# Optimization experiments

Measured on AMD Instinct MI355X. Metric: run time of the kernel, lower is better.

## Reference

```python
import jax, jax.numpy as jnp
import numpy as np
import math

L, E, H, T, B, V = 6, 768, 12, 1024, 4, 256
HS = E // H


def _ln(x, w, b, eps=1e-5):
    mu = jnp.mean(x, axis=-1, keepdims=True)
    var = jnp.mean((x - mu) ** 2, axis=-1, keepdims=True)
    return (x - mu) * jax.lax.rsqrt(var + eps) * w + b


def setup_inputs() -> dict:
    key = jax.random.key(0)
    ks = jax.random.split(key, 12)
    std = 0.02
    inp = {
        "idx": jax.random.randint(ks[0], (B, T), 0, V, dtype=jnp.int64),
        "tok_emb": jax.random.normal(ks[1], (V, E), jnp.float32) * std,
        "pos_emb": jnp.zeros((1, T, E), jnp.float32),
        "ln1_w": jnp.ones((L, E), jnp.float32),
        "ln1_b": jnp.zeros((L, E), jnp.float32),
        "Wq": jax.random.normal(ks[2], (L, E, E), jnp.float32) * std,
        "bq": jnp.zeros((L, E), jnp.float32),
        "Wk": jax.random.normal(ks[3], (L, E, E), jnp.float32) * std,
        "bk": jnp.zeros((L, E), jnp.float32),
        "Wv": jax.random.normal(ks[4], (L, E, E), jnp.float32) * std,
        "bv": jnp.zeros((L, E), jnp.float32),
        "Wp": jax.random.normal(ks[5], (L, E, E), jnp.float32) * std,
        "bp": jnp.zeros((L, E), jnp.float32),
        "ln2_w": jnp.ones((L, E), jnp.float32),
        "ln2_b": jnp.zeros((L, E), jnp.float32),
        "W1": jax.random.normal(ks[6], (L, E, 4 * E), jnp.float32) * std,
        "b1": jnp.zeros((L, 4 * E), jnp.float32),
        "W2": jax.random.normal(ks[7], (L, 4 * E, E), jnp.float32) * std,
        "b2": jnp.zeros((L, E), jnp.float32),
        "lnf_w": jnp.ones((E,), jnp.float32),
        "lnf_b": jnp.zeros((E,), jnp.float32),
        "lm_head": jax.random.normal(ks[8], (E, V), jnp.float32) * std,
    }
    return inp


def reference(idx, tok_emb, pos_emb, ln1_w, ln1_b, Wq, bq, Wk, bk, Wv, bv, Wp, bp,
              ln2_w, ln2_b, W1, b1, W2, b2, lnf_w, lnf_b, lm_head):
    Bc, Tc = idx.shape
    causal = jnp.tril(jnp.ones((Tc, Tc), bool))  # [T,T]
    scale = 1.0 / math.sqrt(HS)
    x = tok_emb[idx] + pos_emb[:, :Tc, :]  # [B,T,E]
    for l in range(L):
        h = _ln(x, ln1_w[l], ln1_b[l])
        q = (h @ Wq[l] + bq[l]).reshape(Bc, Tc, H, HS).transpose(0, 2, 1, 3)
        k = (h @ Wk[l] + bk[l]).reshape(Bc, Tc, H, HS).transpose(0, 2, 1, 3)
        v = (h @ Wv[l] + bv[l]).reshape(Bc, Tc, H, HS).transpose(0, 2, 1, 3)
        att = jnp.einsum('bhtd,bhsd->bhts', q, k) * scale  # [B,H,T,T]
        att = jnp.where(causal, att, -jnp.inf)
        att = jax.nn.softmax(att, axis=-1)
        y = jnp.einsum('bhts,bhsd->bhtd', att, v)
        y = y.transpose(0, 2, 1, 3).reshape(Bc, Tc, E)
        x = x + (y @ Wp[l] + bp[l])
        h2 = _ln(x, ln2_w[l], ln2_b[l])
        m = jax.nn.gelu(h2 @ W1[l] + b1[l], approximate=False)
        x = x + (m @ W2[l] + b2[l])
    x = _ln(x, lnf_w, lnf_b)
    logits = x @ lm_head  # [B,T,V]
    return logits
```

## Files before the change

kernel.cpp:

```cpp
#include <hip/hip_runtime.h>

#define L_ 6
#define E_ 768
#define H_ 12
#define T_ 1024
#define B_ 4
#define V_ 256
#define M_ (B_*T_)
#define E4_ (4*E_)
#define QKVN (3*E_)
#define NZ_ 4

typedef __bf16 bf16;
typedef __bf16 bf16x8 __attribute__((ext_vector_type(8)));
typedef __bf16 bf16x4 __attribute__((ext_vector_type(4)));
typedef float f32x4 __attribute__((ext_vector_type(4)));

#define GF_GELU     1
#define GF_BIAS_EXT 16
#define GF_PART     32

__device__ __forceinline__ float ldf(const void* p, size_t i, int f32m) {
    return f32m ? ((const float*)p)[i] : (float)((const bf16*)p)[i];
}

__device__ __forceinline__ void async_cp16(const void* g, void* l) {
    __builtin_amdgcn_global_load_lds(
        (__attribute__((address_space(1))) void*)g,
        (__attribute__((address_space(3))) void*)l, 16, 0, 0);
}

__device__ __forceinline__ float exp2_hw(float x) {
    float r; asm("v_exp_f32 %0, %1" : "=v"(r) : "v"(x)); return r;
}

__global__ __launch_bounds__(256) void k_probe(const void* __restrict__ tok,
    const void* __restrict__ idxp, int* __restrict__ dm)
{
    __shared__ int sc1, sc2;
    if (threadIdx.x == 0) { sc1 = 0; sc2 = 0; }
    __syncthreads();
    const bf16* tb = (const bf16*)tok;
    int c1 = 0;
    for (int i = threadIdx.x; i < 4096; i += 256) {
        float v = (float)tb[2 * i];
        if (!(fabsf(v) < 100.f)) c1++;
    }
    const int* ip = (const int*)idxp;
    int c2 = 0;
    for (int i = threadIdx.x; i < 1024; i += 256)
        if (ip[2 * i + 1] != 0) c2++;
    atomicAdd(&sc1, c1);
    atomicAdd(&sc2, c2);
    __syncthreads();
    if (threadIdx.x == 0) { dm[0] = (sc1 > 400) ? 1 : 0; dm[1] = (sc2 < 100) ? 1 : 0; }
}

__global__ __launch_bounds__(256) void k_embed(const void* __restrict__ idxp,
    const void* __restrict__ tok, const void* __restrict__ pos,
    float* __restrict__ x, const int* __restrict__ dm)
{
    int f32m = dm[0], i64m = dm[1];
    int bt = blockIdx.x;
    int t  = bt & (T_ - 1);
    int id = i64m ? ((const int*)idxp)[2 * bt] : ((const int*)idxp)[bt];
    float* xo = x + (size_t)bt * E_;
    for (int e = threadIdx.x; e < E_; e += 256)
        xo[e] = ldf(tok, (size_t)id * E_ + e, f32m) + ldf(pos, (size_t)t * E_ + e, f32m);
}

__global__ __launch_bounds__(256) void k_ln(const float* __restrict__ x,
    const void* __restrict__ w, const void* __restrict__ b, size_t wboff,
    bf16* __restrict__ out, const int* __restrict__ dm)
{
    int f32m = dm[0];
    int row = blockIdx.x;
    int tid = threadIdx.x;
    const float* xr = x + (size_t)row * E_;
    float v0 = xr[tid], v1 = xr[tid + 256], v2 = xr[tid + 512];
    float s  = v0 + v1 + v2;
    float s2 = v0*v0 + v1*v1 + v2*v2;
    for (int off = 32; off; off >>= 1) {
        s  += __shfl_xor(s,  off);
        s2 += __shfl_xor(s2, off);
    }
    __shared__ float ls[4], ls2[4];
    int wave = tid >> 6;
    if ((tid & 63) == 0) { ls[wave] = s; ls2[wave] = s2; }
    __syncthreads();
    s  = ls[0] + ls[1] + ls[2] + ls[3];
    s2 = ls2[0] + ls2[1] + ls2[2] + ls2[3];
    float mu  = s * (1.0f / E_);
    float var = s2 * (1.0f / E_) - mu * mu;
    float rs  = rsqrtf(var + 1e-5f);
    bf16* o = out + (size_t)row * E_;
    o[tid]       = (bf16)(((v0 - mu) * rs) * ldf(w, wboff + tid,       f32m) + ldf(b, wboff + tid,       f32m));
    o[tid + 256] = (bf16)(((v1 - mu) * rs) * ldf(w, wboff + tid + 256, f32m) + ldf(b, wboff + tid + 256, f32m));
    o[tid + 512] = (bf16)(((v2 - mu) * rs) * ldf(w, wboff + tid + 512, f32m) + ldf(b, wboff + tid + 512, f32m));
}

__global__ __launch_bounds__(256) void k_red_ln(float* __restrict__ x,
    const float* __restrict__ part,
    const void* __restrict__ gb, size_t gboff,
    const void* __restrict__ w, const void* __restrict__ b, size_t wboff,
    bf16* __restrict__ out, const int* __restrict__ dm)
{
    const size_t PSTR = (size_t)M_ * E_;
    int f32m = dm[0];
    int row = blockIdx.x;
    int tid = threadIdx.x;
    float* xr = x + (size_t)row * E_;
    const float* pr = part + (size_t)row * E_;
    float v[3];
    #pragma unroll
    for (int j = 0; j < 3; j++) {
        int c = tid + j * 256;
        float acc = xr[c];
        #pragma unroll
        for (int z = 0; z < NZ_; z++) acc += pr[(size_t)z * PSTR + c];
        acc += ldf(gb, gboff + c, f32m);
        v[j] = acc;
        xr[c] = acc;
    }
    float s  = v[0] + v[1] + v[2];
    float s2 = v[0]*v[0] + v[1]*v[1] + v[2]*v[2];
    for (int off = 32; off; off >>= 1) {
        s  += __shfl_xor(s,  off);
        s2 += __shfl_xor(s2, off);
    }
    __shared__ float ls[4], ls2[4];
    int wave = tid >> 6;
    if ((tid & 63) == 0) { ls[wave] = s; ls2[wave] = s2; }
    __syncthreads();
    s  = ls[0] + ls[1] + ls[2] + ls[3];
    s2 = ls2[0] + ls2[1] + ls2[2] + ls2[3];
    float mu  = s * (1.0f / E_);
    float var = s2 * (1.0f / E_) - mu * mu;
    float rs  = rsqrtf(var + 1e-5f);
    bf16* o = out + (size_t)row * E_;
    #pragma unroll
    for (int j = 0; j < 3; j++) {
        int c = tid + j * 256;
        o[c] = (bf16)(((v[j] - mu) * rs) * ldf(w, wboff + c, f32m) + ldf(b, wboff + c, f32m));
    }
}

__global__ __launch_bounds__(256) void k_transpose(const void* __restrict__ in, size_t inoff,
    bf16* __restrict__ out, int R, int C, const int* __restrict__ dm)
{
    int f32m = dm[0];
    __shared__ bf16 tile[32][33];
    int r0 = blockIdx.x * 32, c0 = blockIdx.y * 32;
    int tx = threadIdx.x & 31, ty = threadIdx.x >> 5;
    #pragma unroll
    for (int i = 0; i < 4; i++)
        tile[ty + 8*i][tx] = (bf16)ldf(in, inoff + (size_t)(r0 + ty + 8*i) * C + (c0 + tx), f32m);
    __syncthreads();
    #pragma unroll
    for (int i = 0; i < 4; i++)
        out[(size_t)(c0 + ty + 8*i) * R + (r0 + tx)] = tile[tx][ty + 8*i];
}

__global__ __launch_bounds__(256) void k_transpose3(const void* __restrict__ a,
    const void* __restrict__ b, const void* __restrict__ c, size_t inoff,
    bf16* __restrict__ out, int R, int C, const int* __restrict__ dm)
{
    int f32m = dm[0];
    const void* in = (blockIdx.z == 0) ? a : ((blockIdx.z == 1) ? b : c);
    bf16* o = out + (size_t)blockIdx.z * R * C;
    __shared__ bf16 tile[32][33];
    int r0 = blockIdx.x * 32, c0 = blockIdx.y * 32;
    int tx = threadIdx.x & 31, ty = threadIdx.x >> 5;
    #pragma unroll
    for (int i = 0; i < 4; i++)
        tile[ty + 8*i][tx] = (bf16)ldf(in, inoff + (size_t)(r0 + ty + 8*i) * C + (c0 + tx), f32m);
    __syncthreads();
    #pragma unroll
    for (int i = 0; i < 4; i++)
        o[(size_t)(c0 + ty + 8*i) * R + (r0 + tx)] = tile[tx][ty + 8*i];
}

__global__ __launch_bounds__(256) void k_cat3(const void* __restrict__ a,
    const void* __restrict__ b, const void* __restrict__ c, size_t voff,
    bf16* __restrict__ o, const int* __restrict__ dm)
{
    int f32m = dm[0];
    int i = blockIdx.x * 256 + threadIdx.x;
    float v = (i < E_) ? ldf(a, voff + i, f32m)
            : ((i < 2*E_) ? ldf(b, voff + i - E_, f32m) : ldf(c, voff + i - 2*E_, f32m));
    o[i] = (bf16)v;
}

__global__ __launch_bounds__(256) void k_cast_red(const float* __restrict__ in,
    void* __restrict__ out, const int* __restrict__ dm)
{
    const size_t S = (size_t)M_ * V_ / 4;
    size_t i = (size_t)blockIdx.x * 256 + threadIdx.x;
    const f32x4* p = (const f32x4*)in;
    f32x4 v = p[i];
    v += p[S + i];
    v += p[2*S + i];
    v += p[3*S + i];
    if (dm[0]) {
        ((f32x4*)out)[i] = v;
    } else {
        bf16x4 o;
        #pragma unroll
        for (int j = 0; j < 4; j++) o[j] = (bf16)v[j];
        ((bf16x4*)out)[i] = o;
    }
}

__global__ __launch_bounds__(256) void k_gemm(const bf16* __restrict__ A,
    const bf16* __restrict__ BT, const void* __restrict__ bias, size_t boff,
    void* __restrict__ outp, int M, int N, int K, int flags, const int* __restrict__ dm)
{
    int f32m = dm[0];
    __shared__ __attribute__((aligned(16))) bf16 As[128 * 64];
    __shared__ __attribute__((aligned(16))) bf16 Bs[128 * 64];
    int tid = threadIdx.x;
    int bn0 = blockIdx.x * 128, bm0 = blockIdx.y * 128;
    int kz = blockIdx.z;
    int Ks = K / gridDim.z;
    int kbeg = kz * Ks, kend = kbeg + Ks;
    int wave = tid >> 6, lane = tid & 63, quad = lane >> 4, l16 = lane & 15;
    int wr = wave >> 1, wc = wave & 1;

    int st_col = 8 * ((lane & 7) ^ (lane >> 3));
    int st_row_base = wave * 32 + (lane >> 3);

    f32x4 acc[4][4];
    #pragma unroll
    for (int i = 0; i < 4; i++)
        #pragma unroll
        for (int j = 0; j < 4; j++)
            acc[i][j] = (f32x4){0.f, 0.f, 0.f, 0.f};

    int sw = l16 & 7;
    for (int k0 = kbeg; k0 < kend; k0 += 64) {
        #pragma unroll
        for (int i = 0; i < 4; i++) {
            int row = st_row_base + i * 8;
            const bf16* ga = A  + (size_t)(bm0 + row) * K + k0 + st_col;
            const bf16* gb = BT + (size_t)(bn0 + row) * K + k0 + st_col;
            bf16* la = As + (size_t)(wave * 256 + i * 64) * 8;
            bf16* lb = Bs + (size_t)(wave * 256 + i * 64) * 8;
            async_cp16(ga, la);
            async_cp16(gb, lb);
        }
        __syncthreads();
        #pragma unroll
        for (int ks = 0; ks < 2; ks++) {
            bf16x8 af[4], bfr[4];
            #pragma unroll
            for (int mi = 0; mi < 4; mi++) {
                int row = wr*64 + mi*16 + l16;
                int kgs = (4*ks + quad) ^ sw;
                af[mi] = *(const bf16x8*)&As[row*64 + kgs*8];
            }
            #pragma unroll
            for (int ni = 0; ni < 4; ni++) {
                int row = wc*64 + ni*16 + l16;
                int kgs = (4*ks + quad) ^ sw;
                bfr[ni] = *(const bf16x8*)&Bs[row*64 + kgs*8];
            }
            #pragma unroll
            for (int mi = 0; mi < 4; mi++)
                #pragma unroll
                for (int ni = 0; ni < 4; ni++)
                    acc[mi][ni] = __builtin_amdgcn_mfma_f32_16x16x32_bf16(af[mi], bfr[ni], acc[mi][ni], 0, 0, 0);
        }
        __syncthreads();
    }

    float* pout = (float*)outp + (size_t)kz * M * N;
    #pragma unroll
    for (int mi = 0; mi < 4; mi++) {
        #pragma unroll
        for (int ni = 0; ni < 4; ni++) {
            int col = bn0 + wc*64 + ni*16 + l16;
            float bv = 0.f;
            if (bias)
                bv = (flags & GF_BIAS_EXT) ? ldf(bias, boff + col, f32m)
                                           : (float)((const bf16*)bias)[col];
            #pragma unroll
            for (int r = 0; r < 4; r++) {
                int row = bm0 + wr*64 + mi*16 + quad*4 + r;
                float val = acc[mi][ni][r] + bv;
                if (flags & GF_GELU) val = 0.5f * val * (1.f + erff(val * 0.70710678118f));
                size_t oidx = (size_t)row * N + col;
                if (flags & GF_PART) pout[oidx] = val;
                else                 ((bf16*)outp)[oidx] = (bf16)val;
            }
        }
    }
}

__device__ __forceinline__ void attn_qk_softmax2(
    const bf16x8 qf[2], f32x4 OT[4], float& m_ln, float& l_ln,
    const bf16* __restrict__ Kbuf, bf16 (*Ps)[72],
    int wave, int quad, int l16, int s0, int qt0, bool diag)
{
    f32x4 S[4];
    #pragma unroll
    for (int i = 0; i < 4; i++) S[i] = (f32x4){0.f, 0.f, 0.f, 0.f};
    #pragma unroll
    for (int ks = 0; ks < 2; ks++)
        #pragma unroll
        for (int ni = 0; ni < 4; ni++) {
            int kg = (ks*4 + quad) ^ (l16 & 7);
            bf16x8 kf = *(const bf16x8*)&Kbuf[(ni*16 + l16)*64 + kg*8];
            S[ni] = __builtin_amdgcn_mfma_f32_16x16x32_bf16(kf, qf[ks], S[ni], 0, 0, 0);
        }
    const float SC = 0.18033688011112042f;
    if (diag) {
        int qr = qt0 + wave*16 + l16;
        #pragma unroll
        for (int ni = 0; ni < 4; ni++)
            #pragma unroll
            for (int r = 0; r < 4; r++) {
                int scol = s0 + ni*16 + quad*4 + r;
                S[ni][r] = (scol > qr) ? -1e30f : S[ni][r] * SC;
            }
    } else {
        #pragma unroll
        for (int ni = 0; ni < 4; ni++)
            #pragma unroll
            for (int r = 0; r < 4; r++) S[ni][r] *= SC;
    }
    float tn[4];
    #pragma unroll
    for (int ni = 0; ni < 4; ni++)
        tn[ni] = fmaxf(fmaxf(S[ni][0], S[ni][1]), fmaxf(S[ni][2], S[ni][3]));
    float tm = fmaxf(fmaxf(tn[0], tn[1]), fmaxf(tn[2], tn[3]));
    tm = fmaxf(tm, __shfl_xor(tm, 16));
    tm = fmaxf(tm, __shfl_xor(tm, 32));
    float mnew = fmaxf(m_ln, tm);
    float alpha = exp2_hw(m_ln - mnew);
    m_ln = mnew;
    float rsum = 0.f;
    bf16x4 pk[4];
    #pragma unroll
    for (int ni = 0; ni < 4; ni++)
        #pragma unroll
        for (int r = 0; r < 4; r++) {
            float p = exp2_hw(S[ni][r] - mnew);
            rsum += p;
            pk[ni][r] = (bf16)p;
        }
    rsum += __shfl_xor(rsum, 16);
    rsum += __shfl_xor(rsum, 32);
    l_ln = l_ln * alpha + rsum;
    #pragma unroll
    for (int ni = 0; ni < 4; ni++)
        #pragma unroll
        for (int r = 0; r < 4; r++) OT[ni][r] *= alpha;
    #pragma unroll
    for (int ni = 0; ni < 4; ni++)
        *(bf16x4*)&Ps[wave*16 + l16][ni*16 + quad*4] = pk[ni];
}

__device__ __forceinline__ void attn_pv(
    f32x4 OT[4], const bf16 (*Ps)[72], const bf16 (*Vt)[72],
    int wave, int quad, int l16)
{
    #pragma unroll
    for (int ks = 0; ks < 2; ks++) {
        bf16x8 pf = *(const bf16x8*)&Ps[wave*16 + l16][ks*32 + quad*8];
        #pragma unroll
        for (int ni = 0; ni < 4; ni++) {
            bf16x8 vf = *(const bf16x8*)&Vt[ni*16 + l16][ks*32 + quad*8];
            OT[ni] = __builtin_amdgcn_mfma_f32_16x16x32_bf16(vf, pf, OT[ni], 0, 0, 0);
        }
    }
}

__global__ __launch_bounds__(256) void k_attn(const bf16* __restrict__ qkv, bf16* __restrict__ y)
{
    int x = blockIdx.x;
    int qt = x * 64;
    int h = blockIdx.y, b = blockIdx.z;
    int tid = threadIdx.x, wave = tid >> 6, lane = tid & 63, quad = lane >> 4, l16 = lane & 15;

    const bf16* qb = qkv + (size_t)b * T_ * QKVN + h * 64;
    const bf16* kb = qb + E_;
    const bf16* vb = qb + 2 * E_;

    __shared__ __attribute__((aligned(16))) bf16 Kbuf[64 * 64];
    __shared__ __attribute__((aligned(16))) bf16 Vbuf[64 * 64];
    __shared__ __attribute__((aligned(16))) bf16 Vt[64][72];
    __shared__ __attribute__((aligned(16))) bf16 Ps[64][72];

    int srow = tid >> 3;
    int scol = 8 * ((lane & 7) ^ (srow & 7));

    bf16x8 qf[2];
    {
        int qr = qt + wave * 16 + l16;
        #pragma unroll
        for (int ks = 0; ks < 2; ks++)
            qf[ks] = *(const bf16x8*)(qb + (size_t)qr * QKVN + ks*32 + quad*8);
    }

    f32x4 OT[4];
    #pragma unroll
    for (int i = 0; i < 4; i++) OT[i] = (f32x4){0.f,0.f,0.f,0.f};
    float m_ln = -3.0e38f, l_ln = 0.f;

    auto stage = [&](int s0) {
        #pragma unroll
        for (int i = 0; i < 2; i++) {
            int row = i * 32 + srow;
            const bf16* gk = kb + (size_t)(s0 + row) * QKVN + scol;
            const bf16* gv = vb + (size_t)(s0 + row) * QKVN + scol;
            bf16* lk = Kbuf + ((size_t)i * 32 + wave * 8) * 64;
            bf16* lv = Vbuf + ((size_t)i * 32 + wave * 8) * 64;
            async_cp16(gk, lk);
            async_cp16(gv, lv);
        }
    };

    stage(0);
    asm volatile("s_waitcnt vmcnt(0)" ::: "memory");
    __syncthreads();

    for (int st = 0; st <= x; st++) {
        int s0 = st * 64;
        {
            int d = lane;
            int dg = d >> 3, de = d & 7;
            #pragma unroll
            for (int ii = 0; ii < 2; ii++) {
                int sb = wave * 2 + ii;
                bf16x8 tv;
                #pragma unroll
                for (int j = 0; j < 8; j++)
                    tv[j] = Vbuf[(sb*8 + j) * 64 + ((dg ^ j) * 8) + de];
                *(bf16x8*)&Vt[d][sb * 8] = tv;
            }
        }
        attn_qk_softmax2(qf, OT, m_ln, l_ln, Kbuf, Ps, wave, quad, l16, s0, qt, st == x);
        __syncthreads();
        if (st < x) stage(s0 + 64);
        attn_pv(OT, Ps, Vt, wave, quad, l16);
        asm volatile("s_waitcnt vmcnt(0)" ::: "memory");
        __syncthreads();
    }

    float inv = 1.f / l_ln;
    int qrow = qt + wave * 16 + l16;
    #pragma unroll
    for (int ni = 0; ni < 4; ni++) {
        bf16x4 ov;
        #pragma unroll
        for (int r = 0; r < 4; r++) ov[r] = (bf16)(OT[ni][r] * inv);
        *(bf16x4*)&y[(size_t)(b * T_ + qrow) * E_ + h*64 + ni*16 + quad*4] = ov;
    }
}

extern "C" void kernel_launch(void* const* d_in, const int* in_sizes, int n_in,
                              void* d_out, int out_size, void* d_ws, size_t ws_size,
                              hipStream_t stream)
{
    const void* idx     = d_in[0];
    const void* tok_emb = d_in[1];
    const void* pos_emb = d_in[2];
    const void* ln1_w   = d_in[3];
    const void* ln1_b   = d_in[4];
    const void* Wq      = d_in[5];
    const void* bq      = d_in[6];
    const void* Wk      = d_in[7];
    const void* bk      = d_in[8];
    const void* Wv      = d_in[9];
    const void* bv      = d_in[10];
    const void* Wp      = d_in[11];
    const void* bp      = d_in[12];
    const void* ln2_w   = d_in[13];
    const void* ln2_b   = d_in[14];
    const void* W1      = d_in[15];
    const void* b1      = d_in[16];
    const void* W2      = d_in[17];
    const void* b2      = d_in[18];
    const void* lnf_w   = d_in[19];
    const void* lnf_b   = d_in[20];
    const void* lm_head = d_in[21];

    char* base = (char*)d_ws;
    size_t off = 0;
    auto nxt = [&](size_t bytes) -> void* {
        void* p = base + off;
        off += (bytes + 255) & ~(size_t)255;
        return p;
    };
    int*   dm   = (int*)  nxt(256);
    float* x    = (float*)nxt((size_t)M_ * E_ * 4);
    bf16*  h    = (bf16*) nxt((size_t)M_ * E_ * 2);
    bf16*  qkv  = (bf16*) nxt((size_t)M_ * QKVN * 2);
    bf16*  yb   = (bf16*) nxt((size_t)M_ * E_ * 2);
    bf16*  mbuf = (bf16*) nxt((size_t)M_ * E4_ * 2);
    bf16*  wt   = (bf16*) nxt((size_t)E4_ * E_ * 2);
    bf16*  bcat = (bf16*) nxt((size_t)QKVN * 2);
    float* part = (float*)nxt((size_t)NZ_ * M_ * E_ * 4);
    (void)ws_size; (void)in_sizes; (void)n_in; (void)out_size;

    k_probe<<<1, 256, 0, stream>>>(tok_emb, idx, dm);
    k_embed<<<M_, 256, 0, stream>>>(idx, tok_emb, pos_emb, x, dm);

    k_ln<<<M_, 256, 0, stream>>>(x, ln1_w, ln1_b, 0, h, dm);

    for (int l = 0; l < L_; l++) {
        size_t woE  = (size_t)l * E_ * E_;
        size_t voE  = (size_t)l * E_;
        size_t woW1 = (size_t)l * E_ * E4_;
        size_t voE4 = (size_t)l * E4_;

        k_transpose3<<<dim3(E_/32, E_/32, 3), 256, 0, stream>>>(Wq, Wk, Wv, woE, wt, E_, E_, dm);
        k_cat3<<<QKVN/256, 256, 0, stream>>>(bq, bk, bv, voE, bcat, dm);
        k_gemm<<<dim3(QKVN/128, M_/128), 256, 0, stream>>>(h, wt, bcat, 0, qkv, M_, QKVN, E_, 0, dm);

        k_attn<<<dim3(16, H_, B_), 256, 0, stream>>>(qkv, yb);

        k_transpose<<<dim3(E_/32, E_/32), 256, 0, stream>>>(Wp, woE, wt, E_, E_, dm);
        k_gemm<<<dim3(E_/128, M_/128, NZ_), 256, 0, stream>>>(yb, wt, nullptr, 0, part, M_, E_, E_, GF_PART, dm);
        k_red_ln<<<M_, 256, 0, stream>>>(x, part, bp, voE, ln2_w, ln2_b, voE, h, dm);

        k_transpose<<<dim3(E_/32, E4_/32), 256, 0, stream>>>(W1, woW1, wt, E_, E4_, dm);
        k_gemm<<<dim3(E4_/128, M_/128), 256, 0, stream>>>(h, wt, b1, voE4, mbuf, M_, E4_, E_, GF_GELU | GF_BIAS_EXT, dm);

        k_transpose<<<dim3(E4_/32, E_/32), 256, 0, stream>>>(W2, woW1, wt, E4_, E_, dm);
        k_gemm<<<dim3(E_/128, M_/128, NZ_), 256, 0, stream>>>(mbuf, wt, nullptr, 0, part, M_, E_, E4_, GF_PART, dm);
        if (l < L_ - 1)
            k_red_ln<<<M_, 256, 0, stream>>>(x, part, b2, voE, ln1_w, ln1_b, (size_t)(l+1) * E_, h, dm);
        else
            k_red_ln<<<M_, 256, 0, stream>>>(x, part, b2, voE, lnf_w, lnf_b, 0, h, dm);
    }

    k_transpose<<<dim3(E_/32, V_/32), 256, 0, stream>>>(lm_head, 0, wt, E_, V_, dm);
    k_gemm<<<dim3(V_/128, M_/128, NZ_), 256, 0, stream>>>(h, wt, nullptr, 0, part, M_, V_, E_, GF_PART, dm);
    k_cast_red<<<(M_*V_)/1024, 256, 0, stream>>>(part, d_out, dm);
}
```

Measured before the change: 1.463 ms.

## Hoist weight transposes out of layer loop, add 128x64 GEMM, fast GELU

All per-layer weight transposes and bias concatenations now run once before the layer loop, writing into dedicated per-layer buffers instead of a shared scratch buffer. A new 128x64-tile GEMM kernel with split-K of 2 (4 for lm_head) handles the projection, FFN-down and lm_head matmuls, replacing 128x128 tiles with split-K 4. This is meant to cut partial-sum traffic and improve occupancy. GELU now uses a polynomial erf approximation with a hardware exp2 instead of erff, which may change numerical accuracy slightly.

```diff
diff --git a/kernel.cpp b/kernel.cpp
--- a/kernel.cpp
+++ b/kernel.cpp
@@ -9,7 +9,8 @@
 #define M_ (B_*T_)
 #define E4_ (4*E_)
 #define QKVN (3*E_)
-#define NZ_ 4
+#define NZP 2
+#define NZL 4
 
 typedef __bf16 bf16;
 typedef __bf16 bf16x8 __attribute__((ext_vector_type(8)));
@@ -32,6 +33,16 @@
 
 __device__ __forceinline__ float exp2_hw(float x) {
     float r; asm("v_exp_f32 %0, %1" : "=v"(r) : "v"(x)); return r;
+}
+
+__device__ __forceinline__ float gelu_f(float v) {
+    float ax = fabsf(v) * 0.70710678118654752f;
+    float t  = 1.f / (1.f + 0.3275911f * ax);
+    float p  = t*(0.254829592f + t*(-0.284496736f + t*(1.421413741f
+             + t*(-1.453152027f + t*1.061405429f))));
+    float e  = exp2_hw(-1.4426950408889634f * ax * ax);
+    float er = __builtin_copysignf(1.f - p * e, v);
+    return 0.5f * v * (1.f + er);
 }
 
 __global__ __launch_bounds__(256) void k_probe(const void* __restrict__ tok,
@@ -117,7 +128,7 @@
         int c = tid + j * 256;
         float acc = xr[c];
         #pragma unroll
-        for (int z = 0; z < NZ_; z++) acc += pr[(size_t)z * PSTR + c];
+        for (int z = 0; z < NZP; z++) acc += pr[(size_t)z * PSTR + c];
         acc += ldf(gb, gboff + c, f32m);
         v[j] = acc;
         xr[c] = acc;
@@ -145,49 +156,56 @@
     }
 }
 
-__global__ __launch_bounds__(256) void k_transpose(const void* __restrict__ in, size_t inoff,
-    bf16* __restrict__ out, int R, int C, const int* __restrict__ dm)
+__global__ __launch_bounds__(256) void k_transposeZ(const void* __restrict__ in,
+    size_t inoff, size_t zin, bf16* __restrict__ out, size_t zout,
+    int R, int C, const int* __restrict__ dm)
 {
     int f32m = dm[0];
+    __shared__ bf16 tile[32][33];
+    size_t io = inoff + (size_t)blockIdx.z * zin;
+    bf16* o = out + (size_t)blockIdx.z * zout;
+    int r0 = blockIdx.x * 32, c0 = blockIdx.y * 32;
+    int tx = threadIdx.x & 31, ty = threadIdx.x >> 5;
+    #pragma unroll
+    for (int i = 0; i < 4; i++)
+        tile[ty + 8*i][tx] = (bf16)ldf(in, io + (size_t)(r0 + ty + 8*i) * C + (c0 + tx), f32m);
+    __syncthreads();
+    #pragma unroll
+    for (int i = 0; i < 4; i++)
+        o[(size_t)(c0 + ty + 8*i) * R + (r0 + tx)] = tile[tx][ty + 8*i];
+}
+
+__global__ __launch_bounds__(256) void k_transpose3L(const void* __restrict__ a,
+    const void* __restrict__ b, const void* __restrict__ c,
+    bf16* __restrict__ out, const int* __restrict__ dm)
+{
+    int f32m = dm[0];
+    int z = blockIdx.z, l = z / 3, wsel = z - 3 * l;
+    const void* in = (wsel == 0) ? a : ((wsel == 1) ? b : c);
+    size_t io = (size_t)l * E_ * E_;
+    bf16* o = out + (size_t)z * E_ * E_;
     __shared__ bf16 tile[32][33];
     int r0 = blockIdx.x * 32, c0 = blockIdx.y * 32;
     int tx = threadIdx.x & 31, ty = threadIdx.x >> 5;
     #pragma unroll
     for (int i = 0; i < 4; i++)
-        tile[ty + 8*i][tx] = (bf16)ldf(in, inoff + (size_t)(r0 + ty + 8*i) * C + (c0 + tx), f32m);
+        tile[ty + 8*i][tx] = (bf16)ldf(in, io + (size_t)(r0 + ty + 8*i) * E_ + (c0 + tx), f32m);
     __syncthreads();
     #pragma unroll
     for (int i = 0; i < 4; i++)
-        out[(size_t)(c0 + ty + 8*i) * R + (r0 + tx)] = tile[tx][ty + 8*i];
-}
-
-__global__ __launch_bounds__(256) void k_transpose3(const void* __restrict__ a,
-    const void* __restrict__ b, const void* __restrict__ c, size_t inoff,
-    bf16* __restrict__ out, int R, int C, const int* __restrict__ dm)
-{
-    int f32m = dm[0];
-    const void* in = (blockIdx.z == 0) ? a : ((blockIdx.z == 1) ? b : c);
-    bf16* o = out + (size_t)blockIdx.z * R * C;
-    __shared__ bf16 tile[32][33];
-    int r0 = blockIdx.x * 32, c0 = blockIdx.y * 32;
-    int tx = threadIdx.x & 31, ty = threadIdx.x >> 5;
-    #pragma unroll
-    for (int i = 0; i < 4; i++)
-        tile[ty + 8*i][tx] = (bf16)ldf(in, inoff + (size_t)(r0 + ty + 8*i) * C + (c0 + tx), f32m);
-    __syncthreads();
-    #pragma unroll
-    for (int i = 0; i < 4; i++)
-        o[(size_t)(c0 + ty + 8*i) * R + (r0 + tx)] = tile[tx][ty + 8*i];
-}
-
-__global__ __launch_bounds__(256) void k_cat3(const void* __restrict__ a,
-    const void* __restrict__ b, const void* __restrict__ c, size_t voff,
+        o[(size_t)(c0 + ty + 8*i) * E_ + (r0 + tx)] = tile[tx][ty + 8*i];
+}
+
+__global__ __launch_bounds__(256) void k_cat3L(const void* __restrict__ a,
+    const void* __restrict__ b, const void* __restrict__ c,
     bf16* __restrict__ o, const int* __restrict__ dm)
 {
     int f32m = dm[0];
     int i = blockIdx.x * 256 + threadIdx.x;
-    float v = (i < E_) ? ldf(a, voff + i, f32m)
-            : ((i < 2*E_) ? ldf(b, voff + i - E_, f32m) : ldf(c, voff + i - 2*E_, f32m));
+    int l = i / QKVN, j = i - l * QKVN;
+    float v = (j < E_) ? ldf(a, (size_t)l * E_ + j, f32m)
+            : ((j < 2*E_) ? ldf(b, (size_t)l * E_ + j - E_, f32m)
+                          : ldf(c, (size_t)l * E_ + j - 2*E_, f32m));
     o[i] = (bf16)v;
 }
 
@@ -287,7 +305,83 @@
             for (int r = 0; r < 4; r++) {
                 int row = bm0 + wr*64 + mi*16 + quad*4 + r;
                 float val = acc[mi][ni][r] + bv;
-                if (flags & GF_GELU) val = 0.5f * val * (1.f + erff(val * 0.70710678118f));
+                if (flags & GF_GELU) val = gelu_f(val);
+                size_t oidx = (size_t)row * N + col;
+                if (flags & GF_PART) pout[oidx] = val;
+                else                 ((bf16*)outp)[oidx] = (bf16)val;
+            }
+        }
+    }
+}
+
+__global__ __launch_bounds__(256) void k_gemm64(const bf16* __restrict__ A,
+    const bf16* __restrict__ BT, void* __restrict__ outp,
+    int M, int N, int K, int flags, const int* __restrict__ dm)
+{
+    __shared__ __attribute__((aligned(16))) bf16 As[128 * 64];
+    __shared__ __attribute__((aligned(16))) bf16 Bs[64 * 64];
+    int tid = threadIdx.x;
+    int bn0 = blockIdx.x * 64, bm0 = blockIdx.y * 128;
+    int kz = blockIdx.z;
+    int Ks = K / gridDim.z;
+    int kbeg = kz * Ks, kend = kbeg + Ks;
+    int wave = tid >> 6, lane = tid & 63, quad = lane >> 4, l16 = lane & 15;
+    int wr = wave >> 1, wc = wave & 1;
+
+    int st_col = 8 * ((lane & 7) ^ (lane >> 3));
+    int lrow = lane >> 3;
+
+    f32x4 acc[4][2];
+    #pragma unroll
+    for (int i = 0; i < 4; i++)
+        #pragma unroll
+        for (int j = 0; j < 2; j++)
+            acc[i][j] = (f32x4){0.f, 0.f, 0.f, 0.f};
+
+    int sw = l16 & 7;
+    for (int k0 = kbeg; k0 < kend; k0 += 64) {
+        #pragma unroll
+        for (int i = 0; i < 4; i++) {
+            int row = wave * 32 + i * 8 + lrow;
+            async_cp16(A + (size_t)(bm0 + row) * K + k0 + st_col,
+                       As + (size_t)(wave * 32 + i * 8) * 64);
+        }
+        #pragma unroll
+        for (int i = 0; i < 2; i++) {
+            int row = wave * 16 + i * 8 + lrow;
+            async_cp16(BT + (size_t)(bn0 + row) * K + k0 + st_col,
+                       Bs + (size_t)(wave * 16 + i * 8) * 64);
+        }
+        __syncthreads();
+        #pragma unroll
+        for (int ks = 0; ks < 2; ks++) {
+            int kgs = (4*ks + quad) ^ sw;
+            bf16x8 af[4], bfr[2];
+            #pragma unroll
+            for (int mi = 0; mi < 4; mi++)
+                af[mi] = *(const bf16x8*)&As[(wr*64 + mi*16 + l16)*64 + kgs*8];
+            #pragma unroll
+            for (int ni = 0; ni < 2; ni++)
+                bfr[ni] = *(const bf16x8*)&Bs[(wc*32 + ni*16 + l16)*64 + kgs*8];
+            #pragma unroll
+            for (int mi = 0; mi < 4; mi++)
+                #pragma unroll
+                for (int ni = 0; ni < 2; ni++)
+                    acc[mi][ni] = __builtin_amdgcn_mfma_f32_16x16x32_bf16(af[mi], bfr[ni], acc[mi][ni], 0, 0, 0);
+        }
+        __syncthreads();
+    }
+
+    float* pout = (float*)outp + (size_t)kz * M * N;
+    #pragma unroll
+    for (int mi = 0; mi < 4; mi++) {
+        #pragma unroll
+        for (int ni = 0; ni < 2; ni++) {
+            int col = bn0 + wc*32 + ni*16 + l16;
+            #pragma unroll
+            for (int r = 0; r < 4; r++) {
+                int row = bm0 + wr*64 + mi*16 + quad*4 + r;
+                float val = acc[mi][ni][r];
                 size_t oidx = (size_t)row * N + col;
                 if (flags & GF_PART) pout[oidx] = val;
                 else                 ((bf16*)outp)[oidx] = (bf16)val;
@@ -492,50 +586,58 @@
         off += (bytes + 255) & ~(size_t)255;
         return p;
     };
-    int*   dm   = (int*)  nxt(256);
-    float* x    = (float*)nxt((size_t)M_ * E_ * 4);
-    bf16*  h    = (bf16*) nxt((size_t)M_ * E_ * 2);
-    bf16*  qkv  = (bf16*) nxt((size_t)M_ * QKVN * 2);
-    bf16*  yb   = (bf16*) nxt((size_t)M_ * E_ * 2);
-    bf16*  mbuf = (bf16*) nxt((size_t)M_ * E4_ * 2);
-    bf16*  wt   = (bf16*) nxt((size_t)E4_ * E_ * 2);
-    bf16*  bcat = (bf16*) nxt((size_t)QKVN * 2);
-    float* part = (float*)nxt((size_t)NZ_ * M_ * E_ * 4);
+    int*   dm    = (int*)  nxt(256);
+    float* x     = (float*)nxt((size_t)M_ * E_ * 4);
+    bf16*  h     = (bf16*) nxt((size_t)M_ * E_ * 2);
+    bf16*  qkv   = (bf16*) nxt((size_t)M_ * QKVN * 2);
+    bf16*  yb    = (bf16*) nxt((size_t)M_ * E_ * 2);
+    bf16*  mbuf  = (bf16*) nxt((size_t)M_ * E4_ * 2);
+    bf16*  wqkvT = (bf16*) nxt((size_t)L_ * 3 * E_ * E_ * 2);
+    bf16*  wpT   = (bf16*) nxt((size_t)L_ * E_ * E_ * 2);
+    bf16*  w1T   = (bf16*) nxt((size_t)L_ * E_ * E4_ * 2);
+    bf16*  w2T   = (bf16*) nxt((size_t)L_ * E4_ * E_ * 2);
+    bf16*  lmhT  = (bf16*) nxt((size_t)V_ * E_ * 2);
+    bf16*  bcat  = (bf16*) nxt((size_t)L_ * QKVN * 2);
+    float* part  = (float*)nxt((size_t)NZL * M_ * V_ * 4 > (size_t)NZP * M_ * E_ * 4
+                             ? (size_t)NZL * M_ * V_ * 4 : (size_t)NZP * M_ * E_ * 4);
     (void)ws_size; (void)in_sizes; (void)n_in; (void)out_size;
 
     k_probe<<<1, 256, 0, stream>>>(tok_emb, idx, dm);
     k_embed<<<M_, 256, 0, stream>>>(idx, tok_emb, pos_emb, x, dm);
 
+    k_transpose3L<<<dim3(E_/32, E_/32, 3*L_), 256, 0, stream>>>(Wq, Wk, Wv, wqkvT, dm);
+    k_transposeZ<<<dim3(E_/32, E_/32, L_), 256, 0, stream>>>(Wp, 0, (size_t)E_*E_, wpT, (size_t)E_*E_, E_, E_, dm);
+    k_transposeZ<<<dim3(E_/32, E4_/32, L_), 256, 0, stream>>>(W1, 0, (size_t)E_*E4_, w1T, (size_t)E_*E4_, E_, E4_, dm);
+    k_transposeZ<<<dim3(E4_/32, E_/32, L_), 256, 0, stream>>>(W2, 0, (size_t)E_*E4_, w2T, (size_t)E_*E4_, E4_, E_, dm);
+    k_transposeZ<<<dim3(E_/32, V_/32, 1), 256, 0, stream>>>(lm_head, 0, 0, lmhT, 0, E_, V_, dm);
+    k_cat3L<<<(L_*QKVN)/256, 256, 0, stream>>>(bq, bk, bv, bcat, dm);
+
     k_ln<<<M_, 256, 0, stream>>>(x, ln1_w, ln1_b, 0, h, dm);
 
     for (int l = 0; l < L_; l++) {
-        size_t woE  = (size_t)l * E_ * E_;
         size_t voE  = (size_t)l * E_;
-        size_t woW1 = (size_t)l * E_ * E4_;
         size_t voE4 = (size_t)l * E4_;
 
-        k_transpose3<<<dim3(E_/32, E_/32, 3), 256, 0, stream>>>(Wq, Wk, Wv, woE, wt, E_, E_, dm);
-        k_cat3<<<QKVN/256, 256, 0, stream>>>(bq, bk, bv, voE, bcat, dm);
-        k_gemm<<<dim3(QKVN/128, M_/128), 256, 0, stream>>>(h, wt, bcat, 0, qkv, M_, QKVN, E_, 0, dm);
+        k_gemm<<<dim3(QKVN/128, M_/128), 256, 0, stream>>>(h, wqkvT + (size_t)l*3*E_*E_,
+            bcat + (size_t)l*QKVN, 0, qkv, M_, QKVN, E_, 0, dm);
 
         k_attn<<<dim3(16, H_, B_), 256, 0, stream>>>(qkv, yb);
 
-        k_transpose<<<dim3(E_/32, E_/32), 256, 0, stream>>>(Wp, woE, wt, E_, E_, dm);
-        k_gemm<<<dim3(E_/128, M_/128, NZ_), 256, 0, stream>>>(yb, wt, nullptr, 0, part, M_, E_, E_, GF_PART, dm);
+        k_gemm64<<<dim3(E_/64, M_/128, NZP), 256, 0, stream>>>(yb, wpT + (size_t)l*E_*E_,
+            part, M_, E_, E_, GF_PART, dm);
         k_red_ln<<<M_, 256, 0, stream>>>(x, part, bp, voE, ln2_w, ln2_b, voE, h, dm);
 
-        k_transpose<<<dim3(E_/32, E4_/32), 256, 0, stream>>>(W1, woW1, wt, E_, E4_, dm);
-        k_gemm<<<dim3(E4_/128, M_/128), 256, 0, stream>>>(h, wt, b1, voE4, mbuf, M_, E4_, E_, GF_GELU | GF_BIAS_EXT, dm);
-
-        k_transpose<<<dim3(E4_/32, E_/32), 256, 0, stream>>>(W2, woW1, wt, E4_, E_, dm);
-        k_gemm<<<dim3(E_/128, M_/128, NZ_), 256, 0, stream>>>(mbuf, wt, nullptr, 0, part, M_, E_, E4_, GF_PART, dm);
+        k_gemm<<<dim3(E4_/128, M_/128), 256, 0, stream>>>(h, w1T + (size_t)l*E_*E4_,
+            b1, voE4, mbuf, M_, E4_, E_, GF_GELU | GF_BIAS_EXT, dm);
+
+        k_gemm64<<<dim3(E_/64, M_/128, NZP), 256, 0, stream>>>(mbuf, w2T + (size_t)l*E_*E4_,
+            part, M_, E_, E4_, GF_PART, dm);
         if (l < L_ - 1)
             k_red_ln<<<M_, 256, 0, stream>>>(x, part, b2, voE, ln1_w, ln1_b, (size_t)(l+1) * E_, h, dm);
         else
             k_red_ln<<<M_, 256, 0, stream>>>(x, part, b2, voE, lnf_w, lnf_b, 0, h, dm);
     }
 
-    k_transpose<<<dim3(E_/32, V_/32), 256, 0, stream>>>(lm_head, 0, wt, E_, V_, dm);
-    k_gemm<<<dim3(V_/128, M_/128, NZ_), 256, 0, stream>>>(h, wt, nullptr, 0, part, M_, V_, E_, GF_PART, dm);
+    k_gemm64<<<dim3(V_/64, M_/128, NZL), 256, 0, stream>>>(h, lmhT, part, M_, V_, E_, GF_PART, dm);
     k_cast_red<<<(M_*V_)/1024, 256, 0, stream>>>(part, d_out, dm);
 }
```

Measured after the change: 1.366 ms. -6.7%, faster.
